# Optimization experiments

Measured on AMD Instinct MI355X. Metric: run time of the kernel, lower is better.

Reference implementation:

```python
import jax, jax.numpy as jnp
from jax import lax
import numpy as np

B = 8
NUM_ANCHORS = 1047552
PROPOSAL_COUNT = 1000
NMS_THRESHOLD = 0.7
RPN_BBOX_STD_DEV = np.array([0.1, 0.1, 0.2, 0.2], dtype=np.float32)
RPN_NMS_LIMIT = 6000


def setup_inputs() -> dict:
    key = jax.random.key(0)
    k1, k2, k3 = jax.random.split(key, 3)
    rpn_scores = jax.random.uniform(k1, (B, NUM_ANCHORS, 2), dtype=jnp.float32)
    rpn_bbox_delta = jax.random.normal(k2, (B, NUM_ANCHORS, 4), dtype=jnp.float32)
    # Build valid normalized anchors (y1,x1,y2,x2) from uniform randoms.
    u = jax.random.uniform(k3, (NUM_ANCHORS, 4), dtype=jnp.float32)
    cy, cx = u[:, 0], u[:, 1]
    h = u[:, 2] * 0.2 + 0.01
    w = u[:, 3] * 0.2 + 0.01
    anchors = jnp.stack([cy - 0.5 * h, cx - 0.5 * w, cy + 0.5 * h, cx + 0.5 * w], axis=-1)
    anchors = jnp.clip(anchors, 0.0, 1.0)
    return {"rpn_scores": rpn_scores, "rpn_bbox_delta": rpn_bbox_delta, "anchors": anchors}


def _apply_box_deltas(boxes, deltas):
    # boxes: [..., (y1,x1,y2,x2)], deltas: [..., (dy,dx,log(dh),log(dw))]
    h = boxes[..., 2] - boxes[..., 0]
    w = boxes[..., 3] - boxes[..., 1]
    cy = boxes[..., 0] + 0.5 * h + deltas[..., 0] * h
    cx = boxes[..., 1] + 0.5 * w + deltas[..., 1] * w
    h = h * jnp.exp(deltas[..., 2])
    w = w * jnp.exp(deltas[..., 3])
    y1 = cy - 0.5 * h
    x1 = cx - 0.5 * w
    return jnp.stack([y1, x1, y1 + h, x1 + w], axis=-1)


def _nms_indices(boxes):
    # Greedy NMS over boxes already sorted by descending score. boxes: [N,4].
    N = boxes.shape[0]
    areas = (boxes[:, 2] - boxes[:, 0]) * (boxes[:, 3] - boxes[:, 1])

    def body(i, state):
        valid, sel = state
        idx = jnp.argmax(valid)          # first still-valid box = highest score
        has = valid[idx]
        sel = sel.at[i].set(jnp.where(has, idx, -1))
        b = boxes[idx]
        yy1 = jnp.maximum(b[0], boxes[:, 0])
        xx1 = jnp.maximum(b[1], boxes[:, 1])
        yy2 = jnp.minimum(b[2], boxes[:, 2])
        xx2 = jnp.minimum(b[3], boxes[:, 3])
        inter = jnp.maximum(yy2 - yy1, 0.0) * jnp.maximum(xx2 - xx1, 0.0)
        union = areas[idx] + areas - inter
        iou = jnp.where(union > 0, inter / union, 0.0)
        keep = valid & (iou <= NMS_THRESHOLD)
        keep = keep.at[idx].set(False)
        valid = jnp.where(has, keep, valid)
        return valid, sel

    valid0 = jnp.ones((N,), dtype=bool)
    sel0 = jnp.full((PROPOSAL_COUNT,), -1, dtype=jnp.int32)
    _, sel = lax.fori_loop(0, PROPOSAL_COUNT, body, (valid0, sel0))
    return sel


def _nms_single(boxes):
    # boxes: [pre_nms_limit, 4] sorted by score desc -> [proposal_count, 4], zero-padded
    sel = _nms_indices(lax.stop_gradient(boxes))
    props = boxes[jnp.clip(sel, 0)]
    return jnp.where(sel[:, None] >= 0, props, 0.0)


def _forward(rpn_scores, rpn_bbox_delta, anchors):
    scores = rpn_scores[:, :, 1]                                   # [B, A]
    deltas = rpn_bbox_delta * jnp.asarray(RPN_BBOX_STD_DEV)        # [B, A, 4]
    pre_nms_limit = min(RPN_NMS_LIMIT, anchors.shape[0])
    top_scores, ix = lax.top_k(scores, pre_nms_limit)              # [B, pre]
    tgt_deltas = jnp.take_along_axis(deltas, ix[..., None], axis=1)  # [B, pre, 4]
    tgt_anchors = anchors[ix]                                      # [B, pre, 4]
    boxes = _apply_box_deltas(tgt_anchors, tgt_deltas)
    boxes = jnp.clip(boxes, 0.0, 1.0)                              # window (0,0,1,1)
    proposals = jax.vmap(_nms_single)(boxes)                       # [B, proposal_count, 4]
    return proposals


def reference(rpn_scores, rpn_bbox_delta, anchors):
    return _forward(rpn_scores, rpn_bbox_delta, anchors)
```

## Files before the change

### kernel.cpp

```cpp
#include <hip/hip_runtime.h>
#include <stdint.h>

#define NBATCH   8
#define NA       1047552
#define PRE_NMS  6000
#define NPROP    1000
#define BINS     2048
#define HB       64
#define GB       128
#define CAND_CAP 8192
#define NMS_THR  0.7f
#define GBUF     1024
#define SCAP     2048
#define PCHUNK   32
#define PCAP     256
#define REJW     188
#define PTI      64
#define PTJ      1024
#define JR       4
#define KS       8

#define OFF_HIST  ((size_t)0)
#define OFF_BOFF  (OFF_HIST + (size_t)NBATCH*HB*BINS*2)
#define OFF_BCNT  (OFF_BOFF + (size_t)NBATCH*BINS*4)
#define OFF_CTR   (OFF_BCNT + (size_t)NBATCH*BINS*4)
#define CTR_BYTES ((size_t)(32 + NBATCH*PCHUNK*4 + NBATCH*BINS*4))
#define OFF_CAND  (OFF_CTR + 66624)
#define OFF_BOXES (OFF_CAND + (size_t)NBATCH*CAND_CAP*8)
#define OFF_PAIRS (OFF_BOXES + (size_t)NBATCH*PRE_NMS*16)
#define WS_NEEDED (OFF_PAIRS + (size_t)NBATCH*PCHUNK*PCAP*4)

__device__ __forceinline__ unsigned score_bin(float s) {
    int b = (int)(s * (float)BINS);
    if (b < 0) b = 0;
    if (b > BINS - 1) b = BINS - 1;
    return (unsigned)b;
}

__global__ __launch_bounds__(256) void k_hist(const float* __restrict__ scores,
                                              uint16_t* __restrict__ hist) {
    __shared__ uint32_t lh[BINS];
    const int b = blockIdx.y;
    for (int t = threadIdx.x; t < BINS; t += 256) lh[t] = 0;
    __syncthreads();
    const float4* s4 = reinterpret_cast<const float4*>(scores) + (size_t)b * (NA / 2);
    const int n4 = NA / 2;
    const int stride = gridDim.x * 256;
    for (int i = blockIdx.x * 256 + threadIdx.x; i < n4; i += stride) {
        float4 v = s4[i];
        atomicAdd(&lh[score_bin(v.y)], 1u);
        atomicAdd(&lh[score_bin(v.w)], 1u);
    }
    __syncthreads();
    uint16_t* gh = hist + ((size_t)b * HB + blockIdx.x) * BINS;
    for (int t = threadIdx.x; t < BINS; t += 256) gh[t] = (uint16_t)lh[t];
}

__global__ __launch_bounds__(256) void k_hsum(const uint16_t* __restrict__ hist,
                                              uint32_t* __restrict__ bcnt) {
    const int b  = blockIdx.z;
    const int k0 = blockIdx.y * KS;
    const unsigned w = blockIdx.x * 256 + threadIdx.x;
    const uint32_t* hb32 = reinterpret_cast<const uint32_t*>(hist);
    uint32_t s0 = 0, s1 = 0;
    #pragma unroll
    for (int kk = 0; kk < KS; ++kk) {
        uint32_t v = hb32[((size_t)b * HB + (k0 + kk)) * (BINS / 2) + w];
        s0 += v & 0xffffu;
        s1 += v >> 16;
    }
    if (s0) atomicAdd(&bcnt[(size_t)b * BINS + 2 * w], s0);
    if (s1) atomicAdd(&bcnt[(size_t)b * BINS + 2 * w + 1], s1);
}

__global__ __launch_bounds__(256) void k_thresh2(const uint32_t* __restrict__ bcnt,
                                                 uint32_t* __restrict__ boff,
                                                 uint32_t* __restrict__ cbin) {
    __shared__ uint32_t hsum[BINS];
    __shared__ uint32_t csum[256];
    __shared__ int sC;
    const int b = blockIdx.x;
    const int t = threadIdx.x;
    if (t == 0) sC = 0;
    for (int p = t; p < BINS; p += 256) hsum[p] = bcnt[(size_t)b * BINS + p];
    __syncthreads();
    {
        uint32_t c = 0;
        for (int q = 0; q < 8; ++q) c += hsum[t * 8 + q];
        csum[t] = c;
    }
    __syncthreads();
    if (t == 0) {
        uint32_t suf = 0;
        for (int c = 255; c >= 0; --c) { uint32_t v = csum[c]; csum[c] = suf; suf += v; }
    }
    __syncthreads();
    uint32_t acc = csum[t];
    for (int q = 7; q >= 0; --q) {
        int bin = t * 8 + q;
        uint32_t h = hsum[bin];
        boff[(size_t)b * BINS + bin] = acc;
        if (acc + h >= PRE_NMS) atomicMax(&sC, bin);
        acc += h;
    }
    __syncthreads();
    if (t == 0) cbin[b] = (uint32_t)sC;
}

__global__ __launch_bounds__(256) void k_gather(const float* __restrict__ scores,
                                                const uint32_t* __restrict__ cbin,
                                                const uint32_t* __restrict__ boff,
                                                uint32_t* __restrict__ binpos,
                                                uint64_t* __restrict__ cand) {
    __shared__ uint64_t keybuf[GBUF];
    __shared__ uint16_t binbuf[GBUF];
    __shared__ uint32_t bcnts[BINS];
    __shared__ uint32_t gbase[BINS];
    __shared__ uint32_t nbuf;
    const int b = blockIdx.y;
    const unsigned C = cbin[b];
    for (int t = threadIdx.x; t < BINS; t += 256) bcnts[t] = 0;
    if (threadIdx.x == 0) nbuf = 0;
    __syncthreads();
    const float4* s4 = reinterpret_cast<const float4*>(scores) + (size_t)b * (NA / 2);
    const int n4 = NA / 2;
    const int stride = gridDim.x * 256;
    uint64_t* cb = cand + (size_t)b * CAND_CAP;
    for (int i = blockIdx.x * 256 + threadIdx.x; i < n4; i += stride) {
        float4 v = s4[i];
        float sc[2] = { v.y, v.w };
        #pragma unroll
        for (int h = 0; h < 2; ++h) {
            unsigned bin = score_bin(sc[h]);
            if (bin >= C) {
                unsigned idx = 2u * (unsigned)i + (unsigned)h;
                uint64_t key = ((uint64_t)__float_as_uint(sc[h]) << 32) | (uint32_t)(~idx);
                unsigned p = atomicAdd(&nbuf, 1u);
                if (p < GBUF) {
                    keybuf[p] = key; binbuf[p] = (uint16_t)bin;
                    atomicAdd(&bcnts[bin], 1u);
                } else {
                    unsigned pos = boff[(size_t)b * BINS + bin] +
                                   atomicAdd(&binpos[(size_t)b * BINS + bin], 1u);
                    if (pos < CAND_CAP) cb[pos] = key;
                }
            }
        }
    }
    __syncthreads();
    for (int t = threadIdx.x; t < BINS; t += 256) {
        uint32_t c = bcnts[t];
        if (c) gbase[t] = boff[(size_t)b * BINS + t] +
                          atomicAdd(&binpos[(size_t)b * BINS + t], c);
        bcnts[t] = 0;
    }
    __syncthreads();
    unsigned n = nbuf; if (n > GBUF) n = GBUF;
    for (unsigned p = threadIdx.x; p < n; p += 256) {
        unsigned bn = binbuf[p];
        unsigned pos = gbase[bn] + atomicAdd(&bcnts[bn], 1u);
        if (pos < CAND_CAP) cb[pos] = keybuf[p];
    }
}

__global__ __launch_bounds__(256) void k_binsort(const uint32_t* __restrict__ cbin,
                                                 const uint32_t* __restrict__ boff,
                                                 const uint32_t* __restrict__ bcnt,
                                                 uint64_t* __restrict__ cand) {
    __shared__ uint64_t s[SCAP];
    const int b = blockIdx.y;
    const unsigned bin = cbin[b] + blockIdx.x;
    if (bin >= BINS) return;
    unsigned cnt = bcnt[(size_t)b * BINS + bin];
    if (cnt == 0) return;
    unsigned start = boff[(size_t)b * BINS + bin];
    if (start >= CAND_CAP) return;
    if (start + cnt > CAND_CAP) cnt = CAND_CAP - start;
    if (cnt > SCAP) cnt = SCAP;
    unsigned m = 256;
    while (m < cnt) m <<= 1;
    uint64_t* seg = cand + (size_t)b * CAND_CAP + start;
    for (unsigned i = threadIdx.x; i < m; i += 256)
        s[i] = (i < cnt) ? ~seg[i] : ~0ull;
    __syncthreads();
    for (unsigned k = 2; k <= m; k <<= 1) {
        for (unsigned j = k >> 1; j > 0; j >>= 1) {
            for (unsigned i = threadIdx.x; i < m; i += 256) {
                unsigned ixj = i ^ j;
                if (ixj > i) {
                    uint64_t a = s[i], c = s[ixj];
                    bool up = ((i & k) == 0);
                    if ((a > c) == up) { s[i] = c; s[ixj] = a; }
                }
            }
            __syncthreads();
        }
    }
    for (unsigned i = threadIdx.x; i < cnt; i += 256) seg[i] = ~s[i];
}

__global__ __launch_bounds__(256) void k_decode(const uint64_t* __restrict__ cand,
                                                const float* __restrict__ deltas,
                                                const float* __restrict__ anchors,
                                                float4* __restrict__ boxesOut) {
    const int b = blockIdx.y;
    const int r = blockIdx.x * 256 + threadIdx.x;
    if (r >= PRE_NMS) return;
    uint64_t key = cand[(size_t)b * CAND_CAP + r];
    unsigned idx = ~(uint32_t)key;
    float4 o = make_float4(0.f, 0.f, 0.f, 0.f);
    if (idx < NA) {
        float4 a = reinterpret_cast<const float4*>(anchors)[idx];
        float4 d = reinterpret_cast<const float4*>(deltas)[(size_t)b * NA + idx];
        float h = a.z - a.x, w = a.w - a.y;
        float cy = a.x + 0.5f * h + (d.x * 0.1f) * h;
        float cx = a.y + 0.5f * w + (d.y * 0.1f) * w;
        h = h * expf(d.z * 0.2f);
        w = w * expf(d.w * 0.2f);
        float y1 = cy - 0.5f * h, x1 = cx - 0.5f * w;
        float y2 = y1 + h,        x2 = x1 + w;
        o.x = fminf(fmaxf(y1, 0.f), 1.f);
        o.y = fminf(fmaxf(x1, 0.f), 1.f);
        o.z = fminf(fmaxf(y2, 0.f), 1.f);
        o.w = fminf(fmaxf(x2, 0.f), 1.f);
    }
    boxesOut[(size_t)b * PRE_NMS + r] = o;
}

__global__ __launch_bounds__(256) void k_pairs(const float4* __restrict__ boxes,
                                               uint32_t* __restrict__ pcnt,
                                               uint32_t* __restrict__ pairs) {
    const int jb = blockIdx.x;
    const int ib = blockIdx.y;
    const int b  = blockIdx.z;
    const int i0 = ib * PTI;
    const int j0 = jb * PTJ;
    if (i0 > j0 + PTJ - 1) return;
    __shared__ float4 bi[PTI];
    __shared__ float  ai[PTI];
    const int tid = threadIdx.x;
    const float4* bx = boxes + (size_t)b * PRE_NMS;
    const float S = NMS_THR / (1.0f + NMS_THR);
    if (tid < PTI) {
        int ii = i0 + tid;
        float4 v = (ii < PRE_NMS) ? bx[ii] : make_float4(2.f, 2.f, 2.f, 2.f);
        bi[tid] = v;
        ai[tid] = S * ((v.z - v.x) * (v.w - v.y));
    }
    float4 vj[JR]; float aj[JR];
    #pragma unroll
    for (int r = 0; r < JR; ++r) {
        int j = j0 + r * 256 + tid;
        float4 v = (j < PRE_NMS) ? bx[j] : make_float4(2.f, 2.f, 2.f, 2.f);
        vj[r] = v;
        aj[r] = S * ((v.z - v.x) * (v.w - v.y));
    }
    __syncthreads();
    uint32_t* pc = pcnt + b * PCHUNK;
    uint32_t* pb = pairs + (size_t)b * PCHUNK * PCAP;
    const bool touchesDiag = (i0 + PTI - 1 >= j0);
    if (touchesDiag) {
        for (int it = 0; it < PTI; ++it) {
            float4 vi = bi[it];
            float air = ai[it];
            unsigned i = (unsigned)(i0 + it);
            #pragma unroll
            for (int r = 0; r < JR; ++r) {
                float ih = fmaxf(fminf(vj[r].z, vi.z) - fmaxf(vj[r].x, vi.x), 0.f);
                float iw = fmaxf(fminf(vj[r].w, vi.w) - fmaxf(vj[r].y, vi.y), 0.f);
                float inter = ih * iw;
                unsigned j = (unsigned)(j0 + r * 256 + tid);
                if (inter > air + aj[r] && i < j) {
                    unsigned c = (i + j) & (PCHUNK - 1);
                    unsigned pos = atomicAdd(&pc[c], 1u);
                    if (pos < PCAP) pb[(size_t)c * PCAP + pos] = (j << 13) | i;
                }
            }
        }
    } else {
        #pragma unroll 2
        for (int it = 0; it < PTI; ++it) {
            float4 vi = bi[it];
            float air = ai[it];
            #pragma unroll
            for (int r = 0; r < JR; ++r) {
                float ih = fmaxf(fminf(vj[r].z, vi.z) - fmaxf(vj[r].x, vi.x), 0.f);
                float iw = fmaxf(fminf(vj[r].w, vi.w) - fmaxf(vj[r].y, vi.y), 0.f);
                float inter = ih * iw;
                if (inter > air + aj[r]) {
                    unsigned i = (unsigned)(i0 + it);
                    unsigned j = (unsigned)(j0 + r * 256 + tid);
                    unsigned c = (i + j) & (PCHUNK - 1);
                    unsigned pos = atomicAdd(&pc[c], 1u);
                    if (pos < PCAP) pb[(size_t)c * PCAP + pos] = (j << 13) | i;
                }
            }
        }
    }
}

__global__ __launch_bounds__(256) void k_nms_emit(const uint32_t* __restrict__ pcnt,
                                                  const uint32_t* __restrict__ pairsIn,
                                                  const float4* __restrict__ boxes,
                                                  float4* __restrict__ out) {
    __shared__ uint32_t sp[PCHUNK * PCAP];
    __shared__ uint32_t cpref[PCHUNK + 1];
    __shared__ uint32_t rejA[REJW], rejB[REJW], pre[REJW + 1];
    __shared__ int changed;
    const int b = blockIdx.x;
    const int tid = threadIdx.x;
    if (tid == 0) {
        unsigned s = 0;
        for (int c = 0; c < PCHUNK; ++c) {
            cpref[c] = s;
            unsigned cc = pcnt[b * PCHUNK + c];
            if (cc > PCAP) cc = PCAP;
            s += cc;
        }
        cpref[PCHUNK] = s;
    }
    for (int t = tid; t < REJW; t += 256) rejA[t] = 0;
    __syncthreads();
    const unsigned np = cpref[PCHUNK];
    for (int c = 0; c < PCHUNK; ++c) {
        unsigned cnt = cpref[c + 1] - cpref[c];
        for (unsigned k = tid; k < cnt; k += 256)
            sp[cpref[c] + k] = pairsIn[((size_t)b * PCHUNK + c) * PCAP + k];
    }
    __syncthreads();
    for (int iter = 0; iter < PRE_NMS; ++iter) {
        for (int t = tid; t < REJW; t += 256) rejB[t] = 0;
        if (tid == 0) changed = 0;
        __syncthreads();
        for (unsigned p = tid; p < np; p += 256) {
            unsigned u = sp[p];
            unsigned j = u >> 13, i = u & 8191u;
            if (!((rejA[i >> 5] >> (i & 31)) & 1u))
                atomicOr(&rejB[j >> 5], 1u << (j & 31));
        }
        __syncthreads();
        for (int t = tid; t < REJW; t += 256) {
            if (rejB[t] != rejA[t]) changed = 1;
            rejA[t] = rejB[t];
        }
        __syncthreads();
        if (!changed) break;
    }
    if (tid == 0) {
        unsigned c2 = 0;
        for (int w = 0; w < REJW; ++w) { pre[w] = c2; c2 += __popc(rejA[w]); }
        pre[REJW] = c2;
    }
    __syncthreads();
    const float4* bx = boxes + (size_t)b * PRE_NMS;
    float4* ob = out + (size_t)b * NPROP;
    for (int j = tid; j < PRE_NMS; j += 256) {
        unsigned w = (unsigned)j >> 5, bit = (unsigned)j & 31;
        if ((rejA[w] >> bit) & 1u) continue;
        unsigned rank = (unsigned)j - (pre[w] + __popc(rejA[w] & ((1u << bit) - 1u)));
        if (rank < NPROP) ob[rank] = bx[j];
    }
}

extern "C" void kernel_launch(void* const* d_in, const int* in_sizes, int n_in,
                              void* d_out, int out_size, void* d_ws, size_t ws_size,
                              hipStream_t stream) {
    const float* scores  = (const float*)d_in[0];
    const float* deltas  = (const float*)d_in[1];
    const float* anchors = (const float*)d_in[2];

    if (ws_size < WS_NEEDED) return;

    char* ws = (char*)d_ws;
    uint16_t* hist   = (uint16_t*)(ws + OFF_HIST);
    uint32_t* boff   = (uint32_t*)(ws + OFF_BOFF);
    uint32_t* bcnt   = (uint32_t*)(ws + OFF_BCNT);
    uint32_t* cbin   = (uint32_t*)(ws + OFF_CTR);
    uint32_t* pcnt   = cbin + NBATCH;
    uint32_t* binpos = pcnt + NBATCH * PCHUNK;
    uint64_t* cand   = (uint64_t*)(ws + OFF_CAND);
    float4*   boxes  = (float4*)(ws + OFF_BOXES);
    uint32_t* pairs  = (uint32_t*)(ws + OFF_PAIRS);

    hipMemsetAsync((void*)bcnt, 0, (size_t)NBATCH * BINS * 4 + CTR_BYTES, stream);
    hipMemsetAsync(d_out, 0, (size_t)NBATCH * NPROP * 4 * sizeof(float), stream);

    k_hist   <<<dim3(HB, NBATCH), 256, 0, stream>>>(scores, hist);
    k_hsum   <<<dim3(BINS / 512, HB / KS, NBATCH), 256, 0, stream>>>(hist, bcnt);
    k_thresh2<<<NBATCH, 256, 0, stream>>>(bcnt, boff, cbin);
    k_gather <<<dim3(GB, NBATCH), 256, 0, stream>>>(scores, cbin, boff, binpos, cand);
    k_binsort<<<dim3(128, NBATCH), 256, 0, stream>>>(cbin, boff, bcnt, cand);
    k_decode <<<dim3((PRE_NMS + 255) / 256, NBATCH), 256, 0, stream>>>(cand, deltas, anchors, boxes);
    k_pairs  <<<dim3((PRE_NMS + PTJ - 1) / PTJ, (PRE_NMS + PTI - 1) / PTI, NBATCH),
               256, 0, stream>>>(boxes, pcnt, pairs);
    k_nms_emit<<<NBATCH, 256, 0, stream>>>(pcnt, pairs, boxes, (float4*)d_out);
}
```

Before: 393.1 us.

## Fuse hist reduction and box decode, chunk NMS fixpoint by 256-box blocks

The per-block histogram is now atomically added straight into global bin counts, which removes the separate hsum pass. Box decoding is folded into the bin-sort kernel, which also no longer writes sorted keys back to memory. Pairs are bucketed by j>>8 so NMS can resolve suppression chunk by chunk: cross-chunk suppressors are already final, and only intra-chunk dependencies need a local fixpoint over 8 words. This replaces the global iterate-until-stable loop over all pairs. The trade-off is more global atomics in k_hist and a serial pass over chunks in NMS.

```diff
diff --git a/kernel.cpp b/kernel.cpp
--- a/kernel.cpp
+++ b/kernel.cpp
@@ -14,11 +14,10 @@
 #define SCAP     2048
 #define PCHUNK   32
 #define PCAP     256
-#define REJW     188
+#define REJW     192
 #define PTI      64
 #define PTJ      1024
 #define JR       4
-#define KS       8
 
 #define OFF_HIST  ((size_t)0)
 #define OFF_BOFF  (OFF_HIST + (size_t)NBATCH*HB*BINS*2)
@@ -38,7 +37,7 @@
 }
 
 __global__ __launch_bounds__(256) void k_hist(const float* __restrict__ scores,
-                                              uint16_t* __restrict__ hist) {
+                                              uint32_t* __restrict__ bcnt) {
     __shared__ uint32_t lh[BINS];
     const int b = blockIdx.y;
     for (int t = threadIdx.x; t < BINS; t += 256) lh[t] = 0;
@@ -52,25 +51,10 @@
         atomicAdd(&lh[score_bin(v.w)], 1u);
     }
     __syncthreads();
-    uint16_t* gh = hist + ((size_t)b * HB + blockIdx.x) * BINS;
-    for (int t = threadIdx.x; t < BINS; t += 256) gh[t] = (uint16_t)lh[t];
-}
-
-__global__ __launch_bounds__(256) void k_hsum(const uint16_t* __restrict__ hist,
-                                              uint32_t* __restrict__ bcnt) {
-    const int b  = blockIdx.z;
-    const int k0 = blockIdx.y * KS;
-    const unsigned w = blockIdx.x * 256 + threadIdx.x;
-    const uint32_t* hb32 = reinterpret_cast<const uint32_t*>(hist);
-    uint32_t s0 = 0, s1 = 0;
-    #pragma unroll
-    for (int kk = 0; kk < KS; ++kk) {
-        uint32_t v = hb32[((size_t)b * HB + (k0 + kk)) * (BINS / 2) + w];
-        s0 += v & 0xffffu;
-        s1 += v >> 16;
-    }
-    if (s0) atomicAdd(&bcnt[(size_t)b * BINS + 2 * w], s0);
-    if (s1) atomicAdd(&bcnt[(size_t)b * BINS + 2 * w + 1], s1);
+    for (int t = threadIdx.x; t < BINS; t += 256) {
+        uint32_t v = lh[t];
+        if (v) atomicAdd(&bcnt[(size_t)b * BINS + t], v);
+    }
 }
 
 __global__ __launch_bounds__(256) void k_thresh2(const uint32_t* __restrict__ bcnt,
@@ -166,7 +150,10 @@
 __global__ __launch_bounds__(256) void k_binsort(const uint32_t* __restrict__ cbin,
                                                  const uint32_t* __restrict__ boff,
                                                  const uint32_t* __restrict__ bcnt,
-                                                 uint64_t* __restrict__ cand) {
+                                                 const uint64_t* __restrict__ cand,
+                                                 const float* __restrict__ deltas,
+                                                 const float* __restrict__ anchors,
+                                                 float4* __restrict__ boxesOut) {
     __shared__ uint64_t s[SCAP];
     const int b = blockIdx.y;
     const unsigned bin = cbin[b] + blockIdx.x;
@@ -174,12 +161,12 @@
     unsigned cnt = bcnt[(size_t)b * BINS + bin];
     if (cnt == 0) return;
     unsigned start = boff[(size_t)b * BINS + bin];
-    if (start >= CAND_CAP) return;
+    if (start >= PRE_NMS) return;
     if (start + cnt > CAND_CAP) cnt = CAND_CAP - start;
     if (cnt > SCAP) cnt = SCAP;
     unsigned m = 256;
     while (m < cnt) m <<= 1;
-    uint64_t* seg = cand + (size_t)b * CAND_CAP + start;
+    const uint64_t* seg = cand + (size_t)b * CAND_CAP + start;
     for (unsigned i = threadIdx.x; i < m; i += 256)
         s[i] = (i < cnt) ? ~seg[i] : ~0ull;
     __syncthreads();
@@ -196,35 +183,28 @@
             __syncthreads();
         }
     }
-    for (unsigned i = threadIdx.x; i < cnt; i += 256) seg[i] = ~s[i];
-}
-
-__global__ __launch_bounds__(256) void k_decode(const uint64_t* __restrict__ cand,
-                                                const float* __restrict__ deltas,
-                                                const float* __restrict__ anchors,
-                                                float4* __restrict__ boxesOut) {
-    const int b = blockIdx.y;
-    const int r = blockIdx.x * 256 + threadIdx.x;
-    if (r >= PRE_NMS) return;
-    uint64_t key = cand[(size_t)b * CAND_CAP + r];
-    unsigned idx = ~(uint32_t)key;
-    float4 o = make_float4(0.f, 0.f, 0.f, 0.f);
-    if (idx < NA) {
-        float4 a = reinterpret_cast<const float4*>(anchors)[idx];
-        float4 d = reinterpret_cast<const float4*>(deltas)[(size_t)b * NA + idx];
-        float h = a.z - a.x, w = a.w - a.y;
-        float cy = a.x + 0.5f * h + (d.x * 0.1f) * h;
-        float cx = a.y + 0.5f * w + (d.y * 0.1f) * w;
-        h = h * expf(d.z * 0.2f);
-        w = w * expf(d.w * 0.2f);
-        float y1 = cy - 0.5f * h, x1 = cx - 0.5f * w;
-        float y2 = y1 + h,        x2 = x1 + w;
-        o.x = fminf(fmaxf(y1, 0.f), 1.f);
-        o.y = fminf(fmaxf(x1, 0.f), 1.f);
-        o.z = fminf(fmaxf(y2, 0.f), 1.f);
-        o.w = fminf(fmaxf(x2, 0.f), 1.f);
-    }
-    boxesOut[(size_t)b * PRE_NMS + r] = o;
+    for (unsigned i = threadIdx.x; i < cnt; i += 256) {
+        unsigned rank = start + i;
+        if (rank >= PRE_NMS) continue;
+        unsigned idx = (uint32_t)s[i];
+        float4 o = make_float4(0.f, 0.f, 0.f, 0.f);
+        if (idx < NA) {
+            float4 a = reinterpret_cast<const float4*>(anchors)[idx];
+            float4 d = reinterpret_cast<const float4*>(deltas)[(size_t)b * NA + idx];
+            float h = a.z - a.x, w = a.w - a.y;
+            float cy = a.x + 0.5f * h + (d.x * 0.1f) * h;
+            float cx = a.y + 0.5f * w + (d.y * 0.1f) * w;
+            h = h * expf(d.z * 0.2f);
+            w = w * expf(d.w * 0.2f);
+            float y1 = cy - 0.5f * h, x1 = cx - 0.5f * w;
+            float y2 = y1 + h,        x2 = x1 + w;
+            o.x = fminf(fmaxf(y1, 0.f), 1.f);
+            o.y = fminf(fmaxf(x1, 0.f), 1.f);
+            o.z = fminf(fmaxf(y2, 0.f), 1.f);
+            o.w = fminf(fmaxf(x2, 0.f), 1.f);
+        }
+        boxesOut[(size_t)b * PRE_NMS + rank] = o;
+    }
 }
 
 __global__ __launch_bounds__(256) void k_pairs(const float4* __restrict__ boxes,
@@ -271,7 +251,7 @@
                 float inter = ih * iw;
                 unsigned j = (unsigned)(j0 + r * 256 + tid);
                 if (inter > air + aj[r] && i < j) {
-                    unsigned c = (i + j) & (PCHUNK - 1);
+                    unsigned c = j >> 8;
                     unsigned pos = atomicAdd(&pc[c], 1u);
                     if (pos < PCAP) pb[(size_t)c * PCAP + pos] = (j << 13) | i;
                 }
@@ -290,7 +270,7 @@
                 if (inter > air + aj[r]) {
                     unsigned i = (unsigned)(i0 + it);
                     unsigned j = (unsigned)(j0 + r * 256 + tid);
-                    unsigned c = (i + j) & (PCHUNK - 1);
+                    unsigned c = j >> 8;
                     unsigned pos = atomicAdd(&pc[c], 1u);
                     if (pos < PCAP) pb[(size_t)c * PCAP + pos] = (j << 13) | i;
                 }
@@ -305,7 +285,8 @@
                                                   float4* __restrict__ out) {
     __shared__ uint32_t sp[PCHUNK * PCAP];
     __shared__ uint32_t cpref[PCHUNK + 1];
-    __shared__ uint32_t rejA[REJW], rejB[REJW], pre[REJW + 1];
+    __shared__ uint32_t rejA[REJW], pre[REJW + 1];
+    __shared__ uint32_t baseW[8], curW[8], nextW[8];
     __shared__ int changed;
     const int b = blockIdx.x;
     const int tid = threadIdx.x;
@@ -321,30 +302,57 @@
     }
     for (int t = tid; t < REJW; t += 256) rejA[t] = 0;
     __syncthreads();
-    const unsigned np = cpref[PCHUNK];
     for (int c = 0; c < PCHUNK; ++c) {
         unsigned cnt = cpref[c + 1] - cpref[c];
         for (unsigned k = tid; k < cnt; k += 256)
             sp[cpref[c] + k] = pairsIn[((size_t)b * PCHUNK + c) * PCAP + k];
     }
     __syncthreads();
-    for (int iter = 0; iter < PRE_NMS; ++iter) {
-        for (int t = tid; t < REJW; t += 256) rejB[t] = 0;
+    const int NCH = (PRE_NMS + 255) >> 8;
+    for (int c = 0; c < NCH; ++c) {
+        const unsigned lo = cpref[c], hi = cpref[c + 1];
+        if (lo == hi) continue;
         if (tid == 0) changed = 0;
+        if (tid < 8) baseW[tid] = 0;
         __syncthreads();
-        for (unsigned p = tid; p < np; p += 256) {
+        for (unsigned p = lo + tid; p < hi; p += 256) {
             unsigned u = sp[p];
             unsigned j = u >> 13, i = u & 8191u;
-            if (!((rejA[i >> 5] >> (i & 31)) & 1u))
-                atomicOr(&rejB[j >> 5], 1u << (j & 31));
+            if ((int)(i >> 8) == c) {
+                changed = 1;
+            } else if (!((rejA[i >> 5] >> (i & 31)) & 1u)) {
+                atomicOr(&baseW[(j >> 5) & 7], 1u << (j & 31));
+            }
         }
         __syncthreads();
-        for (int t = tid; t < REJW; t += 256) {
-            if (rejB[t] != rejA[t]) changed = 1;
-            rejA[t] = rejB[t];
+        const int hasIn = changed;
+        if (hasIn) {
+            if (tid < 8) curW[tid] = baseW[tid];
+            __syncthreads();
+            for (int it2 = 0; it2 < 256; ++it2) {
+                if (tid == 0) changed = 0;
+                if (tid < 8) nextW[tid] = baseW[tid];
+                __syncthreads();
+                for (unsigned p = lo + tid; p < hi; p += 256) {
+                    unsigned u = sp[p];
+                    unsigned j = u >> 13, i = u & 8191u;
+                    if ((int)(i >> 8) == c &&
+                        !((curW[(i >> 5) & 7] >> (i & 31)) & 1u))
+                        atomicOr(&nextW[(j >> 5) & 7], 1u << (j & 31));
+                }
+                __syncthreads();
+                if (tid < 8) {
+                    if (nextW[tid] != curW[tid]) changed = 1;
+                    curW[tid] = nextW[tid];
+                }
+                __syncthreads();
+                if (!changed) break;
+            }
+            if (tid < 8) rejA[c * 8 + tid] = curW[tid];
+        } else {
+            if (tid < 8) rejA[c * 8 + tid] = baseW[tid];
         }
         __syncthreads();
-        if (!changed) break;
     }
     if (tid == 0) {
         unsigned c2 = 0;
@@ -372,7 +380,6 @@
     if (ws_size < WS_NEEDED) return;
 
     char* ws = (char*)d_ws;
-    uint16_t* hist   = (uint16_t*)(ws + OFF_HIST);
     uint32_t* boff   = (uint32_t*)(ws + OFF_BOFF);
     uint32_t* bcnt   = (uint32_t*)(ws + OFF_BCNT);
     uint32_t* cbin   = (uint32_t*)(ws + OFF_CTR);
@@ -385,12 +392,11 @@
     hipMemsetAsync((void*)bcnt, 0, (size_t)NBATCH * BINS * 4 + CTR_BYTES, stream);
     hipMemsetAsync(d_out, 0, (size_t)NBATCH * NPROP * 4 * sizeof(float), stream);
 
-    k_hist   <<<dim3(HB, NBATCH), 256, 0, stream>>>(scores, hist);
-    k_hsum   <<<dim3(BINS / 512, HB / KS, NBATCH), 256, 0, stream>>>(hist, bcnt);
+    k_hist   <<<dim3(HB, NBATCH), 256, 0, stream>>>(scores, bcnt);
     k_thresh2<<<NBATCH, 256, 0, stream>>>(bcnt, boff, cbin);
     k_gather <<<dim3(GB, NBATCH), 256, 0, stream>>>(scores, cbin, boff, binpos, cand);
-    k_binsort<<<dim3(128, NBATCH), 256, 0, stream>>>(cbin, boff, bcnt, cand);
-    k_decode <<<dim3((PRE_NMS + 255) / 256, NBATCH), 256, 0, stream>>>(cand, deltas, anchors, boxes);
+    k_binsort<<<dim3(128, NBATCH), 256, 0, stream>>>(cbin, boff, bcnt, cand,
+                                                     deltas, anchors, boxes);
     k_pairs  <<<dim3((PRE_NMS + PTJ - 1) / PTJ, (PRE_NMS + PTI - 1) / PTI, NBATCH),
                256, 0, stream>>>(boxes, pcnt, pairs);
     k_nms_emit<<<NBATCH, 256, 0, stream>>>(pcnt, pairs, boxes, (float4*)d_out);
```

Result: slower. 402.1 us (+2.3%).
